# Performance work log

Measured on AMD Instinct MI355X. Metric: run time of the kernel, lower is better.

## Reference

```python
import jax, jax.numpy as jnp
import numpy as np

N = 50000      # total atoms/beads across batch
E = 800000     # total edges (avg degree 16)
H = 128        # hidden_channels
R = 50         # num_rbf
NB = 2         # n_interaction blocks
NG = 64        # num graphs in batch
NT = 100       # num atom types
CUT = 5.0      # upper distance cutoff


def setup_inputs() -> dict:
    key = jax.random.key(0)
    ks = jax.random.split(key, 20)
    atom_types = jax.random.randint(ks[0], (N,), 0, NT)
    pos = jax.random.uniform(ks[1], (N, 3), jnp.float32) * 30.0  # box of 30 Angstrom
    edge_index = jax.random.randint(ks[2], (2, E), 0, N)
    batch = jnp.sort(jax.random.randint(ks[3], (N,), 0, NG))

    def g(k, shape, fan_in):
        return jax.random.normal(k, shape, jnp.float32) * (1.0 / fan_in) ** 0.5

    emb = jax.random.normal(ks[4], (NT, H), jnp.float32) * 0.1
    # filter network per block: Linear(R->H) -> tanh -> Linear(H->H)
    fw1 = g(ks[5], (NB, R, H), R)
    fb1 = jnp.zeros((NB, H), jnp.float32)
    fw2 = g(ks[6], (NB, H, H), H)
    fb2 = jnp.zeros((NB, H), jnp.float32)
    # CFConv lin1 (no bias), lin2 (bias)
    lin1_w = g(ks[7], (NB, H, H), H)
    lin2_w = g(ks[8], (NB, H, H), H)
    lin2_b = jnp.zeros((NB, H), jnp.float32)
    # InteractionBlock output linear
    blk_w = g(ks[9], (NB, H, H), H)
    blk_b = jnp.zeros((NB, H), jnp.float32)
    # output network: Linear(H->H/2) -> tanh -> Linear(H/2->1)
    out_w1 = g(ks[10], (H, H // 2), H)
    out_b1 = jnp.zeros((H // 2,), jnp.float32)
    out_w2 = g(ks[11], (H // 2, 1), H // 2)
    out_b2 = jnp.zeros((1,), jnp.float32)
    return dict(atom_types=atom_types, pos=pos, edge_index=edge_index, batch=batch,
                emb=emb, fw1=fw1, fb1=fb1, fw2=fw2, fb2=fb2,
                lin1_w=lin1_w, lin2_w=lin2_w, lin2_b=lin2_b,
                blk_w=blk_w, blk_b=blk_b,
                out_w1=out_w1, out_b1=out_b1, out_w2=out_w2, out_b2=out_b2)


def reference(atom_types, pos, edge_index, batch, emb, fw1, fb1, fw2, fb2,
              lin1_w, lin2_w, lin2_b, blk_w, blk_b,
              out_w1, out_b1, out_w2, out_b2):
    src, dst = edge_index[0], edge_index[1]
    # pairwise distances along edges (eps keeps sqrt grad finite at coincident points)
    diff = pos[src] - pos[dst]                                  # [E,3]
    d = jnp.sqrt(jnp.sum(diff * diff, axis=-1) + 1e-12)         # [E]
    # Gaussian RBF expansion
    offsets = jnp.linspace(0.0, CUT, R)
    coeff = -0.5 / (offsets[1] - offsets[0]) ** 2
    rbf = jnp.exp(coeff * (d[:, None] - offsets) ** 2)          # [E,R]
    # cosine cutoff envelope
    Cenv = jnp.where(d < CUT, 0.5 * (jnp.cos(d * jnp.pi / CUT) + 1.0), 0.0)  # [E]

    x = emb[atom_types]                                          # [N,H]
    for i in range(NB):
        # filter generation from expanded distances
        W = jnp.tanh(rbf @ fw1[i] + fb1[i]) @ fw2[i] + fb2[i]    # [E,H]
        W = W * Cenv[:, None]
        # CFConv: lin1 -> gather*filter -> scatter-sum -> lin2
        h = x @ lin1_w[i]                                        # [N,H]
        msg = h[src] * W                                         # [E,H]
        agg = jax.ops.segment_sum(msg, dst, num_segments=N)      # [N,H]
        h = agg @ lin2_w[i] + lin2_b[i]
        # InteractionBlock: activation -> lin, residual add in SchNet.forward
        h = jnp.tanh(h)
        x = x + (h @ blk_w[i] + blk_b[i])
    # output network -> per-atom energy, scatter-sum per graph
    e = jnp.tanh(x @ out_w1 + out_b1) @ out_w2 + out_b2          # [N,1]
    energy = jax.ops.segment_sum(e, batch, num_segments=NG)      # [NG,1]
    return energy.flatten()
```

## Files before the change

kernel.cpp:

```cpp
#include <hip/hip_runtime.h>
#include <hip/hip_bf16.h>
#include <math.h>

#define H 128
#define RBF 50
#define CUTF 5.0f
#define PIF 3.14159265358979323846f
#define QT 1024
#define SEG 16

__global__ __launch_bounds__(256) void init_pos_x_kernel(
    const int* __restrict__ atype, const float* __restrict__ emb,
    const float* __restrict__ pos,
    float* __restrict__ x, float4* __restrict__ pos4, int Nn, int XB)
{
    if ((int)blockIdx.x < XB) {
        int idx = blockIdx.x * 256 + threadIdx.x;
        if (idx * 4 >= Nn * H) return;
        int n = idx >> 5;
        int c = (idx & 31) * 4;
        const float4 v = *(const float4*)(emb + atype[n] * H + c);
        *(float4*)(x + n * H + c) = v;
    } else {
        int n = ((int)blockIdx.x - XB) * 256 + threadIdx.x;
        if (n < Nn)
            pos4[n] = make_float4(pos[3 * n], pos[3 * n + 1], pos[3 * n + 2], 0.0f);
    }
}

__global__ __launch_bounds__(256) void edge_prep_kernel(
    const float4* __restrict__ pos4, const int* __restrict__ ei, int E, int CAP,
    int* __restrict__ seg_cnt, int* __restrict__ asrc, int* __restrict__ adst,
    float* __restrict__ ad, int* __restrict__ is_src, int* __restrict__ is_dst)
{
    __shared__ int wtot[4], wbase[4];
    const int tid = threadIdx.x;
    const int lane = tid & 63;
    const int wv = tid >> 6;
    const int gtid = blockIdx.x * 256 + tid;

    int s[4], t[4];
    float d[4];
    bool act[4] = {false, false, false, false};

    const int e0 = gtid * 4;
    if (e0 + 3 < E && (E & 3) == 0) {
        const int4 sv = *(const int4*)(ei + e0);
        const int4 tv = *(const int4*)(ei + E + e0);
        s[0] = sv.x; s[1] = sv.y; s[2] = sv.z; s[3] = sv.w;
        t[0] = tv.x; t[1] = tv.y; t[2] = tv.z; t[3] = tv.w;
        #pragma unroll
        for (int j = 0; j < 4; ++j) {
            float4 ps = pos4[s[j]], pt = pos4[t[j]];
            float dx = ps.x - pt.x, dy = ps.y - pt.y, dz = ps.z - pt.z;
            d[j] = sqrtf(dx * dx + dy * dy + dz * dz + 1e-12f);
            act[j] = (d[j] < CUTF);
        }
    } else if (e0 < E) {
        #pragma unroll
        for (int j = 0; j < 4; ++j) {
            int e = e0 + j;
            if (e < E) {
                s[j] = ei[e]; t[j] = ei[E + e];
                float4 ps = pos4[s[j]], pt = pos4[t[j]];
                float dx = ps.x - pt.x, dy = ps.y - pt.y, dz = ps.z - pt.z;
                d[j] = sqrtf(dx * dx + dy * dy + dz * dz + 1e-12f);
                act[j] = (d[j] < CUTF);
            }
        }
    }

    unsigned long long b[4];
    int mytot = 0;
    #pragma unroll
    for (int j = 0; j < 4; ++j) {
        b[j] = __ballot(act[j]);
        mytot += (int)__popcll(b[j]);
    }
    if (lane == 0) wtot[wv] = mytot;
    __syncthreads();
    if (tid == 0) {
        int t0 = wtot[0], t1 = wtot[1], t2 = wtot[2], t3 = wtot[3];
        int tot = t0 + t1 + t2 + t3;
        int base = 0;
        if (tot) base = atomicAdd(&seg_cnt[blockIdx.x & (SEG - 1)], tot);
        wbase[0] = base; wbase[1] = base + t0;
        wbase[2] = base + t0 + t1; wbase[3] = base + t0 + t1 + t2;
    }
    __syncthreads();

    int run = wbase[wv];
    const int segoff = (int)(blockIdx.x & (SEG - 1)) * CAP;
    const unsigned long long ltm = ((unsigned long long)1 << lane) - 1;
    #pragma unroll
    for (int j = 0; j < 4; ++j) {
        if (act[j]) {
            int p = segoff + run + (int)__popcll(b[j] & ltm);
            asrc[p] = s[j]; adst[p] = t[j]; ad[p] = d[j];
            is_src[s[j]] = 1; is_dst[t[j]] = 1;
        }
        run += (int)__popcll(b[j]);
    }
}

__global__ __launch_bounds__(256) void compact_atoms_kernel(
    const int* __restrict__ is_src, const int* __restrict__ is_dst, int Nn,
    int* __restrict__ cnt4,
    int* __restrict__ src_list, int* __restrict__ dst_list, int* __restrict__ nondst_list)
{
    __shared__ int wtot[3][4], wbase[3][4];
    const int tid = threadIdx.x;
    const int lane = tid & 63;
    const int wv = tid >> 6;
    int n = blockIdx.x * 256 + tid;
    bool v[3] = {false, false, false};
    if (n < Nn) {
        v[0] = is_src[n] != 0;
        v[1] = is_dst[n] != 0;
        v[2] = !v[1];
    }
    unsigned long long b[3];
    #pragma unroll
    for (int l = 0; l < 3; ++l) {
        b[l] = __ballot(v[l]);
        if (lane == 0) wtot[l][wv] = (int)__popcll(b[l]);
    }
    __syncthreads();
    if (tid == 0) {
        #pragma unroll
        for (int l = 0; l < 3; ++l) {
            int t0 = wtot[l][0], t1 = wtot[l][1], t2 = wtot[l][2], t3 = wtot[l][3];
            int tot = t0 + t1 + t2 + t3;
            int base = 0;
            if (tot) base = atomicAdd(cnt4 + 1 + l, tot);
            wbase[l][0] = base; wbase[l][1] = base + t0;
            wbase[l][2] = base + t0 + t1; wbase[l][3] = base + t0 + t1 + t2;
        }
    }
    __syncthreads();
    const unsigned long long ltm = ((unsigned long long)1 << lane) - 1;
    if (v[0]) src_list[wbase[0][wv] + (int)__popcll(b[0] & ltm)] = n;
    if (v[1]) dst_list[wbase[1][wv] + (int)__popcll(b[1] & ltm)] = n;
    if (v[2]) nondst_list[wbase[2][wv] + (int)__popcll(b[2] & ltm)] = n;
}

__global__ __launch_bounds__(256) void filter_table_kernel(
    const float* __restrict__ fw1, const float* __restrict__ fb1,
    const float* __restrict__ fw2, const float* __restrict__ fb2,
    const float* __restrict__ lin2b, const float* __restrict__ blkw,
    const float* __restrict__ blkb,
    float* __restrict__ tab, float* __restrict__ cvec)
{
    const int lane = threadIdx.x & 63;
    const int wid = (blockIdx.x * blockDim.x + threadIdx.x) >> 6;
    const int ntab = 2 * (QT + 1);
    if (wid >= ntab + 2) return;
    const int h0 = lane, h1 = lane + 64;

    if (wid >= ntab) {
        const int blk = wid - ntab;
        const float* bwp = blkw + (size_t)blk * H * H;
        float t0 = tanhf(lin2b[blk * H + h0]);
        float t1 = tanhf(lin2b[blk * H + h1]);
        float a0 = blkb[blk * H + h0], a1 = blkb[blk * H + h1];
        #pragma unroll 8
        for (int k = 0; k < 64; ++k) {
            float bb = __shfl(t0, k, 64);
            a0 = fmaf(bb, bwp[k * H + h0], a0);
            a1 = fmaf(bb, bwp[k * H + h1], a1);
        }
        #pragma unroll 8
        for (int k = 0; k < 64; ++k) {
            float bb = __shfl(t1, k, 64);
            a0 = fmaf(bb, bwp[(64 + k) * H + h0], a0);
            a1 = fmaf(bb, bwp[(64 + k) * H + h1], a1);
        }
        cvec[blk * H + h0] = a0;
        cvec[blk * H + h1] = a1;
        return;
    }

    const int blk = wid / (QT + 1);
    const int q = wid - blk * (QT + 1);
    const float d = (float)q * (CUTF / (float)QT);

    const float* f1 = fw1 + (size_t)blk * RBF * H;
    const float* f2 = fw2 + (size_t)blk * H * H;
    const float step  = CUTF / 49.0f;
    const float coeff = -0.5f / (step * step);

    float cenv = (d < CUTF) ? 0.5f * (cosf(d * (PIF / CUTF)) + 1.0f) : 0.0f;

    float t0 = fb1[blk * H + h0], t1 = fb1[blk * H + h1];
    #pragma unroll
    for (int r = 0; r < RBF; ++r) {
        float u = d - (float)r * step;
        float rb = expf(coeff * u * u);
        t0 = fmaf(rb, f1[r * H + h0], t0);
        t1 = fmaf(rb, f1[r * H + h1], t1);
    }
    t0 = tanhf(t0); t1 = tanhf(t1);

    float w0 = fb2[blk * H + h0], w1v = fb2[blk * H + h1];
    #pragma unroll 8
    for (int k = 0; k < 64; ++k) {
        float bb = __shfl(t0, k, 64);
        w0  = fmaf(bb, f2[k * H + h0], w0);
        w1v = fmaf(bb, f2[k * H + h1], w1v);
    }
    #pragma unroll 8
    for (int k = 0; k < 64; ++k) {
        float bb = __shfl(t1, k, 64);
        w0  = fmaf(bb, f2[(64 + k) * H + h0], w0);
        w1v = fmaf(bb, f2[(64 + k) * H + h1], w1v);
    }
    float* row = tab + ((size_t)blk * (QT + 1) + q) * H;
    row[h0] = w0 * cenv;
    row[h1] = w1v * cenv;
}

__global__ __launch_bounds__(256) void edge_scatter_kernel(
    const int* __restrict__ seg_cnt,
    const int* __restrict__ asrc, const int* __restrict__ adst,
    const float* __restrict__ ad, const float* __restrict__ tab,
    const float* __restrict__ hbuf, float* __restrict__ agg, int CAP)
{
    __shared__ int sbase[SEG + 1];
    const int tid = threadIdx.x;
    if (tid == 0) {
        int run = 0;
        #pragma unroll
        for (int s2 = 0; s2 < SEG; ++s2) { sbase[s2] = run; run += seg_cnt[s2]; }
        sbase[SEG] = run;
    }
    __syncthreads();

    const int lane = tid & 63;
    const int wid = (blockIdx.x * blockDim.x + tid) >> 6;
    const int nw  = (gridDim.x * blockDim.x) >> 6;
    const int total = sbase[SEG];
    const float scale = (float)QT / CUTF;

    for (int i = wid; i < total; i += nw) {
        int seg = 0;
        #pragma unroll
        for (int s2 = 1; s2 < SEG; ++s2) seg += (i >= sbase[s2]) ? 1 : 0;
        int slot = seg * CAP + (i - sbase[seg]);

        int s = asrc[slot], t = adst[slot];
        float p = ad[slot] * scale;
        int i0 = (int)p;
        if (i0 > QT - 1) i0 = QT - 1;
        float f = p - (float)i0;
        const float* r0 = tab + (size_t)i0 * H;
        float wl = fmaf(f, r0[H + lane] - r0[lane], r0[lane]);
        float wh = fmaf(f, r0[H + 64 + lane] - r0[64 + lane], r0[64 + lane]);
        float m0 = hbuf[(size_t)s * H + lane] * wl;
        float m1 = hbuf[(size_t)s * H + 64 + lane] * wh;
        atomicAdd(agg + (size_t)t * H + lane, m0);
        atomicAdd(agg + (size_t)t * H + 64 + lane, m1);
    }
}

#define GB 512
#define ZB 128
__global__ __launch_bounds__(256) void gemm_rows_zero_kernel(
    const float* __restrict__ A, const float* __restrict__ W,
    float* __restrict__ C,
    const int* __restrict__ rows, const int* __restrict__ cntp,
    float* __restrict__ zbuf, const int* __restrict__ zrows,
    const int* __restrict__ zcntp)
{
    __shared__ float As[32][36];
    __shared__ float Ws[32][128];
    __shared__ int rlist[32];

    const int tid = threadIdx.x;

    if (blockIdx.x >= GB) {
        int zcnt = *zcntp;
        int total = zcnt * 32;
        for (int idx = (blockIdx.x - GB) * 256 + tid; idx < total; idx += ZB * 256) {
            int row = idx >> 5, c = (idx & 31) << 2;
            int r = zrows[row];
            *(float4*)(zbuf + (size_t)r * H + c) = make_float4(0.f, 0.f, 0.f, 0.f);
        }
        return;
    }

    const int cnt = *cntp;
    const int r0 = (tid >> 4) * 2;
    const int c0 = (tid & 15) * 4;

    for (int tile = blockIdx.x; tile * 32 < cnt; tile += GB) {
        __syncthreads();
        if (tid < 32) {
            int idx = tile * 32 + tid;
            rlist[tid] = (idx < cnt) ? rows[idx] : -1;
        }
        __syncthreads();

        float acc[2][8];
        #pragma unroll
        for (int j = 0; j < 2; ++j)
            #pragma unroll
            for (int c = 0; c < 8; ++c) acc[j][c] = 0.f;

        for (int kc = 0; kc < H; kc += 32) {
            {
                int lr = tid >> 3;
                int kk = (tid & 7) * 4;
                int r = rlist[lr];
                float4 v = make_float4(0.f, 0.f, 0.f, 0.f);
                if (r >= 0) v = *(const float4*)(A + (size_t)r * H + kc + kk);
                *(float4*)&As[lr][kk] = v;
            }
            {
                int wr = tid >> 5;
                int wc = (tid & 31) * 4;
                #pragma unroll
                for (int p = 0; p < 4; ++p) {
                    int row = wr + p * 8;
                    *(float4*)&Ws[row][wc] = *(const float4*)(W + (size_t)(kc + row) * H + wc);
                }
            }
            __syncthreads();
            #pragma unroll
            for (int k = 0; k < 32; k += 4) {
                float a_[2][4];
                #pragma unroll
                for (int j = 0; j < 2; ++j)
                    *(float4*)a_[j] = *(const float4*)&As[r0 + j][k];
                #pragma unroll
                for (int kk = 0; kk < 4; ++kk) {
                    float4 wlo = *(const float4*)&Ws[k + kk][c0];
                    float4 whi = *(const float4*)&Ws[k + kk][c0 + 64];
                    float w_[8] = {wlo.x, wlo.y, wlo.z, wlo.w, whi.x, whi.y, whi.z, whi.w};
                    #pragma unroll
                    for (int j = 0; j < 2; ++j)
                        #pragma unroll
                        for (int c = 0; c < 8; ++c)
                            acc[j][c] = fmaf(a_[j][kk], w_[c], acc[j][c]);
                }
            }
            __syncthreads();
        }
        #pragma unroll
        for (int j = 0; j < 2; ++j) {
            int r = rlist[r0 + j];
            if (r < 0) continue;
            #pragma unroll
            for (int hh = 0; hh < 2; ++hh) {
                int cb = c0 + hh * 64;
                *(float4*)(C + (size_t)r * H + cb) = make_float4(
                    acc[j][hh * 4 + 0], acc[j][hh * 4 + 1],
                    acc[j][hh * 4 + 2], acc[j][hh * 4 + 3]);
            }
        }
    }
}

#define UB 512
#define AB 256
__global__ __launch_bounds__(256) void update_x_kernel(
    const float* __restrict__ agg, const float* __restrict__ l2w,
    const float* __restrict__ l2b, const float* __restrict__ bw,
    const float* __restrict__ bb, float* __restrict__ x,
    const int* __restrict__ rows, const int* __restrict__ cntp,
    const int* __restrict__ nrows, const int* __restrict__ ncntp,
    const float* __restrict__ cvec)
{
    __shared__ float As[32][36];
    __shared__ float Ws[32][128];
    __shared__ float Tl[32][132];
    __shared__ int rlist[32];

    const int tid = threadIdx.x;

    if (blockIdx.x >= UB) {
        int ncnt = *ncntp;
        int total = ncnt * 32;
        for (int idx = (blockIdx.x - UB) * 256 + tid; idx < total; idx += AB * 256) {
            int row = idx >> 5, c = (idx & 31) << 2;
            int r = nrows[row];
            float4 v = *(const float4*)(x + (size_t)r * H + c);
            float4 cv = *(const float4*)(cvec + c);
            v.x += cv.x; v.y += cv.y; v.z += cv.z; v.w += cv.w;
            *(float4*)(x + (size_t)r * H + c) = v;
        }
        return;
    }

    const int cnt = *cntp;
    const int r0 = (tid >> 4) * 2;
    const int c0 = (tid & 15) * 4;

    for (int tile = blockIdx.x; tile * 32 < cnt; tile += UB) {
        __syncthreads();
        if (tid < 32) {
            int idx = tile * 32 + tid;
            rlist[tid] = (idx < cnt) ? rows[idx] : -1;
        }
        __syncthreads();

        float acc[2][8];
        #pragma unroll
        for (int j = 0; j < 2; ++j)
            #pragma unroll
            for (int c = 0; c < 8; ++c) acc[j][c] = 0.f;

        for (int kc = 0; kc < H; kc += 32) {
            {
                int lr = tid >> 3;
                int kk = (tid & 7) * 4;
                int r = rlist[lr];
                float4 v = make_float4(0.f, 0.f, 0.f, 0.f);
                if (r >= 0) v = *(const float4*)(agg + (size_t)r * H + kc + kk);
                *(float4*)&As[lr][kk] = v;
            }
            {
                int wr = tid >> 5;
                int wc = (tid & 31) * 4;
                #pragma unroll
                for (int p = 0; p < 4; ++p) {
                    int row = wr + p * 8;
                    *(float4*)&Ws[row][wc] = *(const float4*)(l2w + (size_t)(kc + row) * H + wc);
                }
            }
            __syncthreads();
            #pragma unroll
            for (int k = 0; k < 32; k += 4) {
                float a_[2][4];
                #pragma unroll
                for (int j = 0; j < 2; ++j)
                    *(float4*)a_[j] = *(const float4*)&As[r0 + j][k];
                #pragma unroll
                for (int kk = 0; kk < 4; ++kk) {
                    float4 wlo = *(const float4*)&Ws[k + kk][c0];
                    float4 whi = *(const float4*)&Ws[k + kk][c0 + 64];
                    float w_[8] = {wlo.x, wlo.y, wlo.z, wlo.w, whi.x, whi.y, whi.z, whi.w};
                    #pragma unroll
                    for (int j = 0; j < 2; ++j)
                        #pragma unroll
                        for (int c = 0; c < 8; ++c)
                            acc[j][c] = fmaf(a_[j][kk], w_[c], acc[j][c]);
                }
            }
            __syncthreads();
        }
        #pragma unroll
        for (int j = 0; j < 2; ++j) {
            float4 lo, hi;
            lo.x = tanhf(acc[j][0] + l2b[c0]);      lo.y = tanhf(acc[j][1] + l2b[c0 + 1]);
            lo.z = tanhf(acc[j][2] + l2b[c0 + 2]);  lo.w = tanhf(acc[j][3] + l2b[c0 + 3]);
            hi.x = tanhf(acc[j][4] + l2b[c0 + 64]); hi.y = tanhf(acc[j][5] + l2b[c0 + 65]);
            hi.z = tanhf(acc[j][6] + l2b[c0 + 66]); hi.w = tanhf(acc[j][7] + l2b[c0 + 67]);
            *(float4*)&Tl[r0 + j][c0] = lo;
            *(float4*)&Tl[r0 + j][c0 + 64] = hi;
        }

        float acc2[2][8];
        #pragma unroll
        for (int j = 0; j < 2; ++j)
            #pragma unroll
            for (int c = 0; c < 8; ++c) acc2[j][c] = 0.f;

        for (int kc = 0; kc < H; kc += 32) {
            __syncthreads();
            {
                int wr = tid >> 5;
                int wc = (tid & 31) * 4;
                #pragma unroll
                for (int p = 0; p < 4; ++p) {
                    int row = wr + p * 8;
                    *(float4*)&Ws[row][wc] = *(const float4*)(bw + (size_t)(kc + row) * H + wc);
                }
            }
            __syncthreads();
            #pragma unroll
            for (int k = 0; k < 32; k += 4) {
                float a_[2][4];
                #pragma unroll
                for (int j = 0; j < 2; ++j)
                    *(float4*)a_[j] = *(const float4*)&Tl[r0 + j][kc + k];
                #pragma unroll
                for (int kk = 0; kk < 4; ++kk) {
                    float4 wlo = *(const float4*)&Ws[k + kk][c0];
                    float4 whi = *(const float4*)&Ws[k + kk][c0 + 64];
                    float w_[8] = {wlo.x, wlo.y, wlo.z, wlo.w, whi.x, whi.y, whi.z, whi.w};
                    #pragma unroll
                    for (int j = 0; j < 2; ++j)
                        #pragma unroll
                        for (int c = 0; c < 8; ++c)
                            acc2[j][c] = fmaf(a_[j][kk], w_[c], acc2[j][c]);
                }
            }
        }
        #pragma unroll
        for (int j = 0; j < 2; ++j) {
            int r = rlist[r0 + j];
            if (r < 0) continue;
            #pragma unroll
            for (int hh = 0; hh < 2; ++hh) {
                int cb = c0 + hh * 64;
                float4 xv = *(const float4*)(x + (size_t)r * H + cb);
                xv.x += acc2[j][hh * 4 + 0] + bb[cb];
                xv.y += acc2[j][hh * 4 + 1] + bb[cb + 1];
                xv.z += acc2[j][hh * 4 + 2] + bb[cb + 2];
                xv.w += acc2[j][hh * 4 + 3] + bb[cb + 3];
                *(float4*)(x + (size_t)r * H + cb) = xv;
            }
        }
    }
}

__global__ __launch_bounds__(256) void out_head_kernel(
    const float* __restrict__ x, const int* __restrict__ batch,
    const float* __restrict__ w1, const float* __restrict__ b1,
    const float* __restrict__ w2, const float* __restrict__ b2,
    float* __restrict__ energy, int Nn)
{
    __shared__ float As[64][33];
    __shared__ float Ws[32][68];
    __shared__ float e_lds[64];
    __shared__ int   gid_lds[64];

    const int tid = threadIdx.x;
    const int m0 = blockIdx.x * 64;
    const int r0 = (tid >> 4) * 4;
    const int c0 = (tid & 15) * 4;

    float acc[4][4];
    #pragma unroll
    for (int j = 0; j < 4; ++j)
        #pragma unroll
        for (int c = 0; c < 4; ++c) acc[j][c] = 0.0f;

    for (int kc = 0; kc < 128; kc += 32) {
        {
            int r = tid >> 3;
            int kk = (tid & 7) * 4;
            #pragma unroll
            for (int p = 0; p < 2; ++p) {
                int row = r + p * 32;
                float4 v = make_float4(0.f, 0.f, 0.f, 0.f);
                if (m0 + row < Nn) v = *(const float4*)(x + (size_t)(m0 + row) * H + kc + kk);
                As[row][kk] = v.x; As[row][kk + 1] = v.y;
                As[row][kk + 2] = v.z; As[row][kk + 3] = v.w;
            }
        }
        {
            int wr = tid >> 4;
            int wc = (tid & 15) * 4;
            #pragma unroll
            for (int p = 0; p < 2; ++p) {
                int row = wr + p * 16;
                *(float4*)&Ws[row][wc] = *(const float4*)(w1 + (size_t)(kc + row) * 64 + wc);
            }
        }
        __syncthreads();
        #pragma unroll
        for (int k = 0; k < 32; ++k) {
            float a_[4];
            #pragma unroll
            for (int j = 0; j < 4; ++j) a_[j] = As[r0 + j][k];
            float4 wv = *(float4*)&Ws[k][c0];
            float w_[4] = {wv.x, wv.y, wv.z, wv.w};
            #pragma unroll
            for (int j = 0; j < 4; ++j)
                #pragma unroll
                for (int c = 0; c < 4; ++c)
                    acc[j][c] = fmaf(a_[j], w_[c], acc[j][c]);
        }
        __syncthreads();
    }

    const float4 b1v = *(const float4*)(b1 + c0);
    const float4 w2v = *(const float4*)(w2 + c0);
    float ep[4];
    #pragma unroll
    for (int j = 0; j < 4; ++j) {
        float v0 = tanhf(acc[j][0] + b1v.x);
        float v1 = tanhf(acc[j][1] + b1v.y);
        float v2 = tanhf(acc[j][2] + b1v.z);
        float v3 = tanhf(acc[j][3] + b1v.w);
        ep[j] = v0 * w2v.x + v1 * w2v.y + v2 * w2v.z + v3 * w2v.w;
    }
    #pragma unroll
    for (int off = 1; off < 16; off <<= 1) {
        #pragma unroll
        for (int j = 0; j < 4; ++j) ep[j] += __shfl_xor(ep[j], off, 64);
    }
    if ((tid & 15) == 0) {
        const float b2v = b2[0];
        #pragma unroll
        for (int j = 0; j < 4; ++j) e_lds[r0 + j] = ep[j] + b2v;
    }
    if (tid < 64) {
        int row = m0 + tid;
        gid_lds[tid] = (row < Nn) ? batch[row] : -1;
    }
    __syncthreads();

    if (tid == 0) {
        int cur = -1; float sum = 0.0f;
        for (int r = 0; r < 64; ++r) {
            int g = gid_lds[r];
            if (g < 0) continue;
            if (g != cur) {
                if (cur >= 0) atomicAdd(&energy[cur], sum);
                cur = g; sum = 0.0f;
            }
            sum += e_lds[r];
        }
        if (cur >= 0) atomicAdd(&energy[cur], sum);
    }
}

extern "C" void kernel_launch(void* const* d_in, const int* in_sizes, int n_in,
                              void* d_out, int out_size, void* d_ws, size_t ws_size,
                              hipStream_t stream)
{
    const int*   atype = (const int*)  d_in[0];
    const float* pos   = (const float*)d_in[1];
    const int*   ei    = (const int*)  d_in[2];
    const int*   batch = (const int*)  d_in[3];
    const float* emb   = (const float*)d_in[4];
    const float* fw1   = (const float*)d_in[5];
    const float* fb1   = (const float*)d_in[6];
    const float* fw2   = (const float*)d_in[7];
    const float* fb2   = (const float*)d_in[8];
    const float* lin1w = (const float*)d_in[9];
    const float* lin2w = (const float*)d_in[10];
    const float* lin2b = (const float*)d_in[11];
    const float* blkw  = (const float*)d_in[12];
    const float* blkb  = (const float*)d_in[13];
    const float* ow1   = (const float*)d_in[14];
    const float* ob1   = (const float*)d_in[15];
    const float* ow2   = (const float*)d_in[16];
    const float* ob2   = (const float*)d_in[17];

    const int Nn = in_sizes[0];
    const int E  = in_sizes[2] / 2;
    float* energy = (float*)d_out;

    const int eblocks = (E + 1023) / 1024;
    const int bps = (eblocks + SEG - 1) / SEG;
    const int CAP = bps * 1024;
    const int SEGCAP = SEG * CAP;

    char* w = (char*)d_ws;
    int*   cnt  = (int*)w;
    int*   seg_cnt = cnt + 8;
    int*   is_src = (int*)(w + 256);
    int*   is_dst = is_src + Nn;
    float* x    = (float*)(is_dst + Nn);
    float* hbuf = x + (size_t)Nn * H;
    float* agg  = hbuf + (size_t)Nn * H;
    int*   asrc = (int*)(agg + (size_t)Nn * H);
    int*   adst = asrc + SEGCAP;
    float* ad   = (float*)(adst + SEGCAP);
    int*   src_list = (int*)(ad + SEGCAP);
    int*   dst_list = src_list + Nn;
    int*   nondst_list = dst_list + Nn;
    float* cvec = (float*)(nondst_list + Nn);
    float* tab  = cvec + 2 * H;
    float4* pos4 = (float4*)(tab + 2 * (size_t)(QT + 1) * H);

    hipMemsetAsync(cnt, 0, 256 + 2 * (size_t)Nn * sizeof(int), stream);
    hipMemsetAsync(energy, 0, (size_t)out_size * sizeof(float), stream);

    {
        int XB = (Nn * 32 + 255) / 256;
        int PB = (Nn + 255) / 256;
        init_pos_x_kernel<<<XB + PB, 256, 0, stream>>>(atype, emb, pos, x, pos4, Nn, XB);
    }
    edge_prep_kernel<<<eblocks, 256, 0, stream>>>(
        pos4, ei, E, CAP, seg_cnt, asrc, adst, ad, is_src, is_dst);
    compact_atoms_kernel<<<(Nn + 255) / 256, 256, 0, stream>>>(
        is_src, is_dst, Nn, cnt, src_list, dst_list, nondst_list);
    {
        int waves = 2 * (QT + 1) + 2;
        filter_table_kernel<<<(waves + 3) / 4, 256, 0, stream>>>(
            fw1, fb1, fw2, fb2, lin2b, blkw, blkb, tab, cvec);
    }

    for (int i = 0; i < 2; ++i) {
        const float* l1w  = lin1w + (size_t)i * H * H;
        const float* l2w  = lin2w + (size_t)i * H * H;
        const float* l2b  = lin2b + (size_t)i * H;
        const float* bw   = blkw + (size_t)i * H * H;
        const float* bb   = blkb + (size_t)i * H;
        const float* tabi = tab + (size_t)i * (QT + 1) * H;

        gemm_rows_zero_kernel<<<GB + ZB, 256, 0, stream>>>(
            x, l1w, hbuf, src_list, cnt + 1, agg, dst_list, cnt + 2);
        edge_scatter_kernel<<<1024, 256, 0, stream>>>(seg_cnt, asrc, adst, ad,
                                                      tabi, hbuf, agg, CAP);
        update_x_kernel<<<UB + AB, 256, 0, stream>>>(
            agg, l2w, l2b, bw, bb, x, dst_list, cnt + 2,
            nondst_list, cnt + 3, cvec + i * H);
    }

    out_head_kernel<<<(Nn + 63) / 64, 256, 0, stream>>>(x, batch, ow1, ob1, ow2, ob2, energy, Nn);
}
```

Before: 250.7 us.

## Specialize atoms by edge role and precompute per-type energies for edgeless atoms

Atoms that never receive edges get a closed-form state, so their output energy is precomputed per atom type in a merged prep kernel. Only destination atoms go through the output head, fused into the final update kernel. Block 0 reads embeddings directly instead of materializing x. The memsets, embedding init and filter-table kernels merge into one prep launch, and the per-graph energy sum uses a binary search over the sorted batch instead of atomics. This removes launches and full-N passes, at the cost of more complex, role-specific code paths.

```diff
diff --git a/kernel.cpp b/kernel.cpp
--- a/kernel.cpp
+++ b/kernel.cpp
@@ -9,23 +9,139 @@
 #define QT 1024
 #define SEG 16
 
-__global__ __launch_bounds__(256) void init_pos_x_kernel(
-    const int* __restrict__ atype, const float* __restrict__ emb,
-    const float* __restrict__ pos,
-    float* __restrict__ x, float4* __restrict__ pos4, int Nn, int XB)
+__global__ __launch_bounds__(256) void prep_kernel(
+    const float* __restrict__ pos, float4* __restrict__ pos4, int Nn,
+    int4* __restrict__ zbase, int zquads,
+    const float* __restrict__ fw1, const float* __restrict__ fb1,
+    const float* __restrict__ fw2, const float* __restrict__ fb2,
+    const float* __restrict__ lin2b, const float* __restrict__ blkw,
+    const float* __restrict__ blkb, const float* __restrict__ emb,
+    const float* __restrict__ ow1, const float* __restrict__ ob1,
+    const float* __restrict__ ow2, const float* __restrict__ ob2,
+    float* __restrict__ tab, float* __restrict__ cvec,
+    float* __restrict__ e_type, int NT,
+    int ZFB, int PB, int FB)
 {
-    if ((int)blockIdx.x < XB) {
-        int idx = blockIdx.x * 256 + threadIdx.x;
-        if (idx * 4 >= Nn * H) return;
-        int n = idx >> 5;
-        int c = (idx & 31) * 4;
-        const float4 v = *(const float4*)(emb + atype[n] * H + c);
-        *(float4*)(x + n * H + c) = v;
-    } else {
-        int n = ((int)blockIdx.x - XB) * 256 + threadIdx.x;
+    int b = blockIdx.x;
+    const int tid = threadIdx.x;
+    const int lane = tid & 63;
+
+    if (b < ZFB) {
+        int i = b * 256 + tid;
+        if (i < zquads) zbase[i] = make_int4(0, 0, 0, 0);
+        return;
+    }
+    b -= ZFB;
+    if (b < PB) {
+        int n = b * 256 + tid;
         if (n < Nn)
             pos4[n] = make_float4(pos[3 * n], pos[3 * n + 1], pos[3 * n + 2], 0.0f);
-    }
+        return;
+    }
+    b -= PB;
+    const int h0 = lane, h1 = lane + 64;
+    if (b < FB) {
+        const int wid = b * 4 + (tid >> 6);
+        const int ntab = 2 * (QT + 1);
+        if (wid >= ntab + 2) return;
+        if (wid >= ntab) {
+            const int blk = wid - ntab;
+            const float* bwp = blkw + (size_t)blk * H * H;
+            float t0 = tanhf(lin2b[blk * H + h0]);
+            float t1 = tanhf(lin2b[blk * H + h1]);
+            float a0 = blkb[blk * H + h0], a1 = blkb[blk * H + h1];
+            #pragma unroll 8
+            for (int k = 0; k < 64; ++k) {
+                float bb2 = __shfl(t0, k, 64);
+                a0 = fmaf(bb2, bwp[k * H + h0], a0);
+                a1 = fmaf(bb2, bwp[k * H + h1], a1);
+            }
+            #pragma unroll 8
+            for (int k = 0; k < 64; ++k) {
+                float bb2 = __shfl(t1, k, 64);
+                a0 = fmaf(bb2, bwp[(64 + k) * H + h0], a0);
+                a1 = fmaf(bb2, bwp[(64 + k) * H + h1], a1);
+            }
+            cvec[blk * H + h0] = a0;
+            cvec[blk * H + h1] = a1;
+            return;
+        }
+        const int blk = wid / (QT + 1);
+        const int q = wid - blk * (QT + 1);
+        const float d = (float)q * (CUTF / (float)QT);
+        const float* f1 = fw1 + (size_t)blk * RBF * H;
+        const float* f2 = fw2 + (size_t)blk * H * H;
+        const float step  = CUTF / 49.0f;
+        const float coeff = -0.5f / (step * step);
+        float cenv = (d < CUTF) ? 0.5f * (cosf(d * (PIF / CUTF)) + 1.0f) : 0.0f;
+
+        float t0 = fb1[blk * H + h0], t1 = fb1[blk * H + h1];
+        #pragma unroll
+        for (int r = 0; r < RBF; ++r) {
+            float u = d - (float)r * step;
+            float rb = expf(coeff * u * u);
+            t0 = fmaf(rb, f1[r * H + h0], t0);
+            t1 = fmaf(rb, f1[r * H + h1], t1);
+        }
+        t0 = tanhf(t0); t1 = tanhf(t1);
+        float w0 = fb2[blk * H + h0], w1v = fb2[blk * H + h1];
+        #pragma unroll 8
+        for (int k = 0; k < 64; ++k) {
+            float bb2 = __shfl(t0, k, 64);
+            w0  = fmaf(bb2, f2[k * H + h0], w0);
+            w1v = fmaf(bb2, f2[k * H + h1], w1v);
+        }
+        #pragma unroll 8
+        for (int k = 0; k < 64; ++k) {
+            float bb2 = __shfl(t1, k, 64);
+            w0  = fmaf(bb2, f2[(64 + k) * H + h0], w0);
+            w1v = fmaf(bb2, f2[(64 + k) * H + h1], w1v);
+        }
+        float* row = tab + ((size_t)blk * (QT + 1) + q) * H;
+        row[h0] = w0 * cenv;
+        row[h1] = w1v * cenv;
+        return;
+    }
+    b -= FB;
+    const int ty = b * 4 + (tid >> 6);
+    if (ty >= NT) return;
+    float xt0 = emb[(size_t)ty * H + h0];
+    float xt1 = emb[(size_t)ty * H + h1];
+    #pragma unroll
+    for (int blk = 0; blk < 2; ++blk) {
+        const float* bwp = blkw + (size_t)blk * H * H;
+        float t0 = tanhf(lin2b[blk * H + h0]);
+        float t1 = tanhf(lin2b[blk * H + h1]);
+        float a0 = blkb[blk * H + h0], a1 = blkb[blk * H + h1];
+        #pragma unroll 8
+        for (int k = 0; k < 64; ++k) {
+            float bb2 = __shfl(t0, k, 64);
+            a0 = fmaf(bb2, bwp[k * H + h0], a0);
+            a1 = fmaf(bb2, bwp[k * H + h1], a1);
+        }
+        #pragma unroll 8
+        for (int k = 0; k < 64; ++k) {
+            float bb2 = __shfl(t1, k, 64);
+            a0 = fmaf(bb2, bwp[(64 + k) * H + h0], a0);
+            a1 = fmaf(bb2, bwp[(64 + k) * H + h1], a1);
+        }
+        xt0 += a0; xt1 += a1;
+    }
+    float y = ob1[lane];
+    #pragma unroll 8
+    for (int k = 0; k < 64; ++k) {
+        float bb2 = __shfl(xt0, k, 64);
+        y = fmaf(bb2, ow1[k * 64 + lane], y);
+    }
+    #pragma unroll 8
+    for (int k = 0; k < 64; ++k) {
+        float bb2 = __shfl(xt1, k, 64);
+        y = fmaf(bb2, ow1[(64 + k) * 64 + lane], y);
+    }
+    y = tanhf(y) * ow2[lane];
+    #pragma unroll
+    for (int off = 32; off; off >>= 1) y += __shfl_xor(y, off, 64);
+    if (lane == 0) e_type[ty] = y + ob2[0];
 }
 
 __global__ __launch_bounds__(256) void edge_prep_kernel(
@@ -106,7 +222,7 @@
 __global__ __launch_bounds__(256) void compact_atoms_kernel(
     const int* __restrict__ is_src, const int* __restrict__ is_dst, int Nn,
     int* __restrict__ cnt4,
-    int* __restrict__ src_list, int* __restrict__ dst_list, int* __restrict__ nondst_list)
+    int* __restrict__ src_list, int* __restrict__ dst_list, int* __restrict__ sn_list)
 {
     __shared__ int wtot[3][4], wbase[3][4];
     const int tid = threadIdx.x;
@@ -117,7 +233,7 @@
     if (n < Nn) {
         v[0] = is_src[n] != 0;
         v[1] = is_dst[n] != 0;
-        v[2] = !v[1];
+        v[2] = v[0] && !v[1];
     }
     unsigned long long b[3];
     #pragma unroll
@@ -141,82 +257,7 @@
     const unsigned long long ltm = ((unsigned long long)1 << lane) - 1;
     if (v[0]) src_list[wbase[0][wv] + (int)__popcll(b[0] & ltm)] = n;
     if (v[1]) dst_list[wbase[1][wv] + (int)__popcll(b[1] & ltm)] = n;
-    if (v[2]) nondst_list[wbase[2][wv] + (int)__popcll(b[2] & ltm)] = n;
-}
-
-__global__ __launch_bounds__(256) void filter_table_kernel(
-    const float* __restrict__ fw1, const float* __restrict__ fb1,
-    const float* __restrict__ fw2, const float* __restrict__ fb2,
-    const float* __restrict__ lin2b, const float* __restrict__ blkw,
-    const float* __restrict__ blkb,
-    float* __restrict__ tab, float* __restrict__ cvec)
-{
-    const int lane = threadIdx.x & 63;
-    const int wid = (blockIdx.x * blockDim.x + threadIdx.x) >> 6;
-    const int ntab = 2 * (QT + 1);
-    if (wid >= ntab + 2) return;
-    const int h0 = lane, h1 = lane + 64;
-
-    if (wid >= ntab) {
-        const int blk = wid - ntab;
-        const float* bwp = blkw + (size_t)blk * H * H;
-        float t0 = tanhf(lin2b[blk * H + h0]);
-        float t1 = tanhf(lin2b[blk * H + h1]);
-        float a0 = blkb[blk * H + h0], a1 = blkb[blk * H + h1];
-        #pragma unroll 8
-        for (int k = 0; k < 64; ++k) {
-            float bb = __shfl(t0, k, 64);
-            a0 = fmaf(bb, bwp[k * H + h0], a0);
-            a1 = fmaf(bb, bwp[k * H + h1], a1);
-        }
-        #pragma unroll 8
-        for (int k = 0; k < 64; ++k) {
-            float bb = __shfl(t1, k, 64);
-            a0 = fmaf(bb, bwp[(64 + k) * H + h0], a0);
-            a1 = fmaf(bb, bwp[(64 + k) * H + h1], a1);
-        }
-        cvec[blk * H + h0] = a0;
-        cvec[blk * H + h1] = a1;
-        return;
-    }
-
-    const int blk = wid / (QT + 1);
-    const int q = wid - blk * (QT + 1);
-    const float d = (float)q * (CUTF / (float)QT);
-
-    const float* f1 = fw1 + (size_t)blk * RBF * H;
-    const float* f2 = fw2 + (size_t)blk * H * H;
-    const float step  = CUTF / 49.0f;
-    const float coeff = -0.5f / (step * step);
-
-    float cenv = (d < CUTF) ? 0.5f * (cosf(d * (PIF / CUTF)) + 1.0f) : 0.0f;
-
-    float t0 = fb1[blk * H + h0], t1 = fb1[blk * H + h1];
-    #pragma unroll
-    for (int r = 0; r < RBF; ++r) {
-        float u = d - (float)r * step;
-        float rb = expf(coeff * u * u);
-        t0 = fmaf(rb, f1[r * H + h0], t0);
-        t1 = fmaf(rb, f1[r * H + h1], t1);
-    }
-    t0 = tanhf(t0); t1 = tanhf(t1);
-
-    float w0 = fb2[blk * H + h0], w1v = fb2[blk * H + h1];
-    #pragma unroll 8
-    for (int k = 0; k < 64; ++k) {
-        float bb = __shfl(t0, k, 64);
-        w0  = fmaf(bb, f2[k * H + h0], w0);
-        w1v = fmaf(bb, f2[k * H + h1], w1v);
-    }
-    #pragma unroll 8
-    for (int k = 0; k < 64; ++k) {
-        float bb = __shfl(t1, k, 64);
-        w0  = fmaf(bb, f2[(64 + k) * H + h0], w0);
-        w1v = fmaf(bb, f2[(64 + k) * H + h1], w1v);
-    }
-    float* row = tab + ((size_t)blk * (QT + 1) + q) * H;
-    row[h0] = w0 * cenv;
-    row[h1] = w1v * cenv;
+    if (v[2]) sn_list[wbase[2][wv] + (int)__popcll(b[2] & ltm)] = n;
 }
 
 __global__ __launch_bounds__(256) void edge_scatter_kernel(
@@ -265,7 +306,8 @@
 #define GB 512
 #define ZB 128
 __global__ __launch_bounds__(256) void gemm_rows_zero_kernel(
-    const float* __restrict__ A, const float* __restrict__ W,
+    const float* __restrict__ A, const int* __restrict__ atype,
+    const float* __restrict__ emb, const float* __restrict__ W,
     float* __restrict__ C,
     const int* __restrict__ rows, const int* __restrict__ cntp,
     float* __restrict__ zbuf, const int* __restrict__ zrows,
@@ -273,7 +315,7 @@
 {
     __shared__ float As[32][36];
     __shared__ float Ws[32][128];
-    __shared__ int rlist[32];
+    __shared__ int rlist[32], tlist[32];
 
     const int tid = threadIdx.x;
 
@@ -296,7 +338,9 @@
         __syncthreads();
         if (tid < 32) {
             int idx = tile * 32 + tid;
-            rlist[tid] = (idx < cnt) ? rows[idx] : -1;
+            int r = (idx < cnt) ? rows[idx] : -1;
+            rlist[tid] = r;
+            tlist[tid] = (atype && r >= 0) ? atype[r] : 0;
         }
         __syncthreads();
 
@@ -312,7 +356,11 @@
                 int kk = (tid & 7) * 4;
                 int r = rlist[lr];
                 float4 v = make_float4(0.f, 0.f, 0.f, 0.f);
-                if (r >= 0) v = *(const float4*)(A + (size_t)r * H + kc + kk);
+                if (r >= 0) {
+                    const float* base = atype ? (emb + (size_t)tlist[lr] * H)
+                                              : (A + (size_t)r * H);
+                    v = *(const float4*)(base + kc + kk);
+                }
                 *(float4*)&As[lr][kk] = v;
             }
             {
@@ -361,32 +409,34 @@
 }
 
 #define UB 512
-#define AB 256
-__global__ __launch_bounds__(256) void update_x_kernel(
+#define AB 128
+__global__ __launch_bounds__(256) void update_x0_kernel(
     const float* __restrict__ agg, const float* __restrict__ l2w,
     const float* __restrict__ l2b, const float* __restrict__ bw,
     const float* __restrict__ bb, float* __restrict__ x,
+    const float* __restrict__ emb, const int* __restrict__ atype,
     const int* __restrict__ rows, const int* __restrict__ cntp,
-    const int* __restrict__ nrows, const int* __restrict__ ncntp,
-    const float* __restrict__ cvec)
+    const int* __restrict__ snrows, const int* __restrict__ sncntp,
+    const float* __restrict__ cvec0)
 {
     __shared__ float As[32][36];
     __shared__ float Ws[32][128];
     __shared__ float Tl[32][132];
-    __shared__ int rlist[32];
+    __shared__ int rlist[32], tlist[32];
 
     const int tid = threadIdx.x;
 
     if (blockIdx.x >= UB) {
-        int ncnt = *ncntp;
+        int ncnt = *sncntp;
         int total = ncnt * 32;
         for (int idx = (blockIdx.x - UB) * 256 + tid; idx < total; idx += AB * 256) {
             int row = idx >> 5, c = (idx & 31) << 2;
-            int r = nrows[row];
-            float4 v = *(const float4*)(x + (size_t)r * H + c);
-            float4 cv = *(const float4*)(cvec + c);
-            v.x += cv.x; v.y += cv.y; v.z += cv.z; v.w += cv.w;
-            *(float4*)(x + (size_t)r * H + c) = v;
+            int r = snrows[row];
+            int ty = atype[r];
+            float4 ev = *(const float4*)(emb + (size_t)ty * H + c);
+            float4 cv = *(const float4*)(cvec0 + c);
+            ev.x += cv.x; ev.y += cv.y; ev.z += cv.z; ev.w += cv.w;
+            *(float4*)(x + (size_t)r * H + c) = ev;
         }
         return;
     }
@@ -399,7 +449,9 @@
         __syncthreads();
         if (tid < 32) {
             int idx = tile * 32 + tid;
-            rlist[tid] = (idx < cnt) ? rows[idx] : -1;
+            int r = (idx < cnt) ? rows[idx] : -1;
+            rlist[tid] = r;
+            tlist[tid] = (r >= 0) ? atype[r] : 0;
         }
         __syncthreads();
 
@@ -500,10 +552,11 @@
         for (int j = 0; j < 2; ++j) {
             int r = rlist[r0 + j];
             if (r < 0) continue;
+            int ty = tlist[r0 + j];
             #pragma unroll
             for (int hh = 0; hh < 2; ++hh) {
                 int cb = c0 + hh * 64;
-                float4 xv = *(const float4*)(x + (size_t)r * H + cb);
+                float4 xv = *(const float4*)(emb + (size_t)ty * H + cb);
                 xv.x += acc2[j][hh * 4 + 0] + bb[cb];
                 xv.y += acc2[j][hh * 4 + 1] + bb[cb + 1];
                 xv.z += acc2[j][hh * 4 + 2] + bb[cb + 2];
@@ -514,107 +567,225 @@
     }
 }
 
-__global__ __launch_bounds__(256) void out_head_kernel(
-    const float* __restrict__ x, const int* __restrict__ batch,
-    const float* __restrict__ w1, const float* __restrict__ b1,
-    const float* __restrict__ w2, const float* __restrict__ b2,
-    float* __restrict__ energy, int Nn)
+__global__ __launch_bounds__(256) void update_e_kernel(
+    const float* __restrict__ agg, const float* __restrict__ l2w,
+    const float* __restrict__ l2b, const float* __restrict__ bw,
+    const float* __restrict__ bb, const float* __restrict__ x,
+    const float* __restrict__ ow1, const float* __restrict__ ob1,
+    const float* __restrict__ ow2, const float* __restrict__ ob2,
+    float* __restrict__ e_atom,
+    const int* __restrict__ rows, const int* __restrict__ cntp)
 {
-    __shared__ float As[64][33];
-    __shared__ float Ws[32][68];
-    __shared__ float e_lds[64];
-    __shared__ int   gid_lds[64];
+    __shared__ float As[32][36];
+    __shared__ float Ws[32][128];
+    __shared__ float Tl[32][132];
+    __shared__ int rlist[32];
 
     const int tid = threadIdx.x;
-    const int m0 = blockIdx.x * 64;
-    const int r0 = (tid >> 4) * 4;
+    const int cnt = *cntp;
+    const int r0 = (tid >> 4) * 2;
     const int c0 = (tid & 15) * 4;
 
-    float acc[4][4];
+    for (int tile = blockIdx.x; tile * 32 < cnt; tile += gridDim.x) {
+        __syncthreads();
+        if (tid < 32) {
+            int idx = tile * 32 + tid;
+            rlist[tid] = (idx < cnt) ? rows[idx] : -1;
+        }
+        __syncthreads();
+
+        float acc[2][8];
+        #pragma unroll
+        for (int j = 0; j < 2; ++j)
+            #pragma unroll
+            for (int c = 0; c < 8; ++c) acc[j][c] = 0.f;
+
+        for (int kc = 0; kc < H; kc += 32) {
+            {
+                int lr = tid >> 3;
+                int kk = (tid & 7) * 4;
+                int r = rlist[lr];
+                float4 v = make_float4(0.f, 0.f, 0.f, 0.f);
+                if (r >= 0) v = *(const float4*)(agg + (size_t)r * H + kc + kk);
+                *(float4*)&As[lr][kk] = v;
+            }
+            {
+                int wr = tid >> 5;
+                int wc = (tid & 31) * 4;
+                #pragma unroll
+                for (int p = 0; p < 4; ++p) {
+                    int row = wr + p * 8;
+                    *(float4*)&Ws[row][wc] = *(const float4*)(l2w + (size_t)(kc + row) * H + wc);
+                }
+            }
+            __syncthreads();
+            #pragma unroll
+            for (int k = 0; k < 32; k += 4) {
+                float a_[2][4];
+                #pragma unroll
+                for (int j = 0; j < 2; ++j)
+                    *(float4*)a_[j] = *(const float4*)&As[r0 + j][k];
+                #pragma unroll
+                for (int kk = 0; kk < 4; ++kk) {
+                    float4 wlo = *(const float4*)&Ws[k + kk][c0];
+                    float4 whi = *(const float4*)&Ws[k + kk][c0 + 64];
+                    float w_[8] = {wlo.x, wlo.y, wlo.z, wlo.w, whi.x, whi.y, whi.z, whi.w};
+                    #pragma unroll
+                    for (int j = 0; j < 2; ++j)
+                        #pragma unroll
+                        for (int c = 0; c < 8; ++c)
+                            acc[j][c] = fmaf(a_[j][kk], w_[c], acc[j][c]);
+                }
+            }
+            __syncthreads();
+        }
+        #pragma unroll
+        for (int j = 0; j < 2; ++j) {
+            float4 lo, hi;
+            lo.x = tanhf(acc[j][0] + l2b[c0]);      lo.y = tanhf(acc[j][1] + l2b[c0 + 1]);
+            lo.z = tanhf(acc[j][2] + l2b[c0 + 2]);  lo.w = tanhf(acc[j][3] + l2b[c0 + 3]);
+            hi.x = tanhf(acc[j][4] + l2b[c0 + 64]); hi.y = tanhf(acc[j][5] + l2b[c0 + 65]);
+            hi.z = tanhf(acc[j][6] + l2b[c0 + 66]); hi.w = tanhf(acc[j][7] + l2b[c0 + 67]);
+            *(float4*)&Tl[r0 + j][c0] = lo;
+            *(float4*)&Tl[r0 + j][c0 + 64] = hi;
+        }
+
+        float acc2[2][8];
+        #pragma unroll
+        for (int j = 0; j < 2; ++j)
+            #pragma unroll
+            for (int c = 0; c < 8; ++c) acc2[j][c] = 0.f;
+
+        for (int kc = 0; kc < H; kc += 32) {
+            __syncthreads();
+            {
+                int wr = tid >> 5;
+                int wc = (tid & 31) * 4;
+                #pragma unroll
+                for (int p = 0; p < 4; ++p) {
+                    int row = wr + p * 8;
+                    *(float4*)&Ws[row][wc] = *(const float4*)(bw + (size_t)(kc + row) * H + wc);
+                }
+            }
+            __syncthreads();
+            #pragma unroll
+            for (int k = 0; k < 32; k += 4) {
+                float a_[2][4];
+                #pragma unroll
+                for (int j = 0; j < 2; ++j)
+                    *(float4*)a_[j] = *(const float4*)&Tl[r0 + j][kc + k];
+                #pragma unroll
+                for (int kk = 0; kk < 4; ++kk) {
+                    float4 wlo = *(const float4*)&Ws[k + kk][c0];
+                    float4 whi = *(const float4*)&Ws[k + kk][c0 + 64];
+                    float w_[8] = {wlo.x, wlo.y, wlo.z, wlo.w, whi.x, whi.y, whi.z, whi.w};
+                    #pragma unroll
+                    for (int j = 0; j < 2; ++j)
+                        #pragma unroll
+                        for (int c = 0; c < 8; ++c)
+                            acc2[j][c] = fmaf(a_[j][kk], w_[c], acc2[j][c]);
+                }
+            }
+        }
+        __syncthreads();
+        #pragma unroll
+        for (int j = 0; j < 2; ++j) {
+            int r = rlist[r0 + j];
+            #pragma unroll
+            for (int hh = 0; hh < 2; ++hh) {
+                int cb = c0 + hh * 64;
+                float4 xv = make_float4(0.f, 0.f, 0.f, 0.f);
+                if (r >= 0) xv = *(const float4*)(x + (size_t)r * H + cb);
+                xv.x += acc2[j][hh * 4 + 0] + bb[cb];
+                xv.y += acc2[j][hh * 4 + 1] + bb[cb + 1];
+                xv.z += acc2[j][hh * 4 + 2] + bb[cb + 2];
+                xv.w += acc2[j][hh * 4 + 3] + bb[cb + 3];
+                *(float4*)&Tl[r0 + j][cb] = xv;
+            }
+        }
+
+        float acc3[2][4];
+        #pragma unroll
+        for (int j = 0; j < 2; ++j)
+            #pragma unroll
+            for (int c = 0; c < 4; ++c) acc3[j][c] = 0.f;
+
+        for (int kc = 0; kc < H; kc += 32) {
+            __syncthreads();
+            {
+                int wr = tid >> 4;
+                int wc = (tid & 15) * 4;
+                #pragma unroll
+                for (int p = 0; p < 2; ++p) {
+                    int row = wr + p * 16;
+                    *(float4*)&Ws[row][wc] = *(const float4*)(ow1 + (size_t)(kc + row) * 64 + wc);
+                }
+            }
+            __syncthreads();
+            #pragma unroll
+            for (int k = 0; k < 32; ++k) {
+                float a_[2];
+                #pragma unroll
+                for (int j = 0; j < 2; ++j) a_[j] = Tl[r0 + j][kc + k];
+                float4 wv = *(const float4*)&Ws[k][c0];
+                #pragma unroll
+                for (int j = 0; j < 2; ++j) {
+                    acc3[j][0] = fmaf(a_[j], wv.x, acc3[j][0]);
+                    acc3[j][1] = fmaf(a_[j], wv.y, acc3[j][1]);
+                    acc3[j][2] = fmaf(a_[j], wv.z, acc3[j][2]);
+                    acc3[j][3] = fmaf(a_[j], wv.w, acc3[j][3]);
+                }
+            }
+        }
+        const float4 b1v = *(const float4*)(ob1 + c0);
+        const float4 w2v = *(const float4*)(ow2 + c0);
+        float ep[2];
+        #pragma unroll
+        for (int j = 0; j < 2; ++j) {
+            float v0 = tanhf(acc3[j][0] + b1v.x);
+            float v1 = tanhf(acc3[j][1] + b1v.y);
+            float v2 = tanhf(acc3[j][2] + b1v.z);
+            float v3 = tanhf(acc3[j][3] + b1v.w);
+            ep[j] = v0 * w2v.x + v1 * w2v.y + v2 * w2v.z + v3 * w2v.w;
+        }
+        #pragma unroll
+        for (int off = 1; off < 16; off <<= 1) {
+            ep[0] += __shfl_xor(ep[0], off, 64);
+            ep[1] += __shfl_xor(ep[1], off, 64);
+        }
+        if ((tid & 15) == 0) {
+            const float b2v = ob2[0];
+            #pragma unroll
+            for (int j = 0; j < 2; ++j) {
+                int r = rlist[r0 + j];
+                if (r >= 0) e_atom[r] = ep[j] + b2v;
+            }
+        }
+    }
+}
+
+__global__ __launch_bounds__(256) void energy_graph_kernel(
+    const int* __restrict__ batch, const int* __restrict__ atype,
+    const int* __restrict__ is_dst, const float* __restrict__ e_atom,
+    const float* __restrict__ e_type, float* __restrict__ energy, int Nn)
+{
+    const int g = blockIdx.x;
+    int lo = 0, hi = Nn;
+    while (lo < hi) { int m = (lo + hi) >> 1; if (batch[m] < g) lo = m + 1; else hi = m; }
+    const int start = lo;
+    hi = Nn;
+    while (lo < hi) { int m = (lo + hi) >> 1; if (batch[m] < g + 1) lo = m + 1; else hi = m; }
+    const int end = lo;
+
+    float s = 0.0f;
+    for (int n = start + (int)threadIdx.x; n < end; n += 256)
+        s += is_dst[n] ? e_atom[n] : e_type[atype[n]];
     #pragma unroll
-    for (int j = 0; j < 4; ++j)
-        #pragma unroll
-        for (int c = 0; c < 4; ++c) acc[j][c] = 0.0f;
-
-    for (int kc = 0; kc < 128; kc += 32) {
-        {
-            int r = tid >> 3;
-            int kk = (tid & 7) * 4;
-            #pragma unroll
-            for (int p = 0; p < 2; ++p) {
-                int row = r + p * 32;
-                float4 v = make_float4(0.f, 0.f, 0.f, 0.f);
-                if (m0 + row < Nn) v = *(const float4*)(x + (size_t)(m0 + row) * H + kc + kk);
-                As[row][kk] = v.x; As[row][kk + 1] = v.y;
-                As[row][kk + 2] = v.z; As[row][kk + 3] = v.w;
-            }
-        }
-        {
-            int wr = tid >> 4;
-            int wc = (tid & 15) * 4;
-            #pragma unroll
-            for (int p = 0; p < 2; ++p) {
-                int row = wr + p * 16;
-                *(float4*)&Ws[row][wc] = *(const float4*)(w1 + (size_t)(kc + row) * 64 + wc);
-            }
-        }
-        __syncthreads();
-        #pragma unroll
-        for (int k = 0; k < 32; ++k) {
-            float a_[4];
-            #pragma unroll
-            for (int j = 0; j < 4; ++j) a_[j] = As[r0 + j][k];
-            float4 wv = *(float4*)&Ws[k][c0];
-            float w_[4] = {wv.x, wv.y, wv.z, wv.w};
-            #pragma unroll
-            for (int j = 0; j < 4; ++j)
-                #pragma unroll
-                for (int c = 0; c < 4; ++c)
-                    acc[j][c] = fmaf(a_[j], w_[c], acc[j][c]);
-        }
-        __syncthreads();
-    }
-
-    const float4 b1v = *(const float4*)(b1 + c0);
-    const float4 w2v = *(const float4*)(w2 + c0);
-    float ep[4];
-    #pragma unroll
-    for (int j = 0; j < 4; ++j) {
-        float v0 = tanhf(acc[j][0] + b1v.x);
-        float v1 = tanhf(acc[j][1] + b1v.y);
-        float v2 = tanhf(acc[j][2] + b1v.z);
-        float v3 = tanhf(acc[j][3] + b1v.w);
-        ep[j] = v0 * w2v.x + v1 * w2v.y + v2 * w2v.z + v3 * w2v.w;
-    }
-    #pragma unroll
-    for (int off = 1; off < 16; off <<= 1) {
-        #pragma unroll
-        for (int j = 0; j < 4; ++j) ep[j] += __shfl_xor(ep[j], off, 64);
-    }
-    if ((tid & 15) == 0) {
-        const float b2v = b2[0];
-        #pragma unroll
-        for (int j = 0; j < 4; ++j) e_lds[r0 + j] = ep[j] + b2v;
-    }
-    if (tid < 64) {
-        int row = m0 + tid;
-        gid_lds[tid] = (row < Nn) ? batch[row] : -1;
-    }
+    for (int off = 32; off; off >>= 1) s += __shfl_xor(s, off, 64);
+    __shared__ float wp[4];
+    if ((threadIdx.x & 63) == 0) wp[threadIdx.x >> 6] = s;
     __syncthreads();
-
-    if (tid == 0) {
-        int cur = -1; float sum = 0.0f;
-        for (int r = 0; r < 64; ++r) {
-            int g = gid_lds[r];
-            if (g < 0) continue;
-            if (g != cur) {
-                if (cur >= 0) atomicAdd(&energy[cur], sum);
-                cur = g; sum = 0.0f;
-            }
-            sum += e_lds[r];
-        }
-        if (cur >= 0) atomicAdd(&energy[cur], sum);
-    }
+    if (threadIdx.x == 0) energy[g] = wp[0] + wp[1] + wp[2] + wp[3];
 }
 
 extern "C" void kernel_launch(void* const* d_in, const int* in_sizes, int n_in,
@@ -642,6 +813,7 @@
 
     const int Nn = in_sizes[0];
     const int E  = in_sizes[2] / 2;
+    const int NT = in_sizes[4] / H;
     float* energy = (float*)d_out;
 
     const int eblocks = (E + 1023) / 1024;
@@ -652,7 +824,7 @@
     char* w = (char*)d_ws;
     int*   cnt  = (int*)w;
     int*   seg_cnt = cnt + 8;
-    int*   is_src = (int*)(w + 256);
+    int*   is_src = cnt + 32;
     int*   is_dst = is_src + Nn;
     float* x    = (float*)(is_dst + Nn);
     float* hbuf = x + (size_t)Nn * H;
@@ -662,45 +834,47 @@
     float* ad   = (float*)(adst + SEGCAP);
     int*   src_list = (int*)(ad + SEGCAP);
     int*   dst_list = src_list + Nn;
-    int*   nondst_list = dst_list + Nn;
-    float* cvec = (float*)(nondst_list + Nn);
+    int*   sn_list  = dst_list + Nn;
+    float* cvec = (float*)(sn_list + Nn);
     float* tab  = cvec + 2 * H;
-    float4* pos4 = (float4*)(tab + 2 * (size_t)(QT + 1) * H);
-
-    hipMemsetAsync(cnt, 0, 256 + 2 * (size_t)Nn * sizeof(int), stream);
-    hipMemsetAsync(energy, 0, (size_t)out_size * sizeof(float), stream);
-
-    {
-        int XB = (Nn * 32 + 255) / 256;
-        int PB = (Nn + 255) / 256;
-        init_pos_x_kernel<<<XB + PB, 256, 0, stream>>>(atype, emb, pos, x, pos4, Nn, XB);
-    }
+    float* e_type = tab + 2 * (size_t)(QT + 1) * H;
+    float* e_atom = e_type + 128;
+    float4* pos4 = (float4*)(e_atom + Nn);
+
+    const int zquads = (128 + 2 * Nn * 4) / 16;
+    const int ZFB = (zquads + 255) / 256;
+    const int PB  = (Nn + 255) / 256;
+    const int FB  = (2 * (QT + 1) + 2 + 3) / 4;
+    const int TB  = (NT + 3) / 4;
+
+    prep_kernel<<<ZFB + PB + FB + TB, 256, 0, stream>>>(
+        pos, pos4, Nn, (int4*)cnt, zquads,
+        fw1, fb1, fw2, fb2, lin2b, blkw, blkb, emb,
+        ow1, ob1, ow2, ob2, tab, cvec, e_type, NT, ZFB, PB, FB);
+
     edge_prep_kernel<<<eblocks, 256, 0, stream>>>(
         pos4, ei, E, CAP, seg_cnt, asrc, adst, ad, is_src, is_dst);
     compact_atoms_kernel<<<(Nn + 255) / 256, 256, 0, stream>>>(
-        is_src, is_dst, Nn, cnt, src_list, dst_list, nondst_list);
-    {
-        int waves = 2 * (QT + 1) + 2;
-        filter_table_kernel<<<(waves + 3) / 4, 256, 0, stream>>>(
-            fw1, fb1, fw2, fb2, lin2b, blkw, blkb, tab, cvec);
-    }
-
-    for (int i = 0; i < 2; ++i) {
-        const float* l1w  = lin1w + (size_t)i * H * H;
-        const float* l2w  = lin2w + (size_t)i * H * H;
-        const float* l2b  = lin2b + (size_t)i * H;
-        const float* bw   = blkw + (size_t)i * H * H;
-        const float* bb   = blkb + (size_t)i * H;
-        const float* tabi = tab + (size_t)i * (QT + 1) * H;
-
-        gemm_rows_zero_kernel<<<GB + ZB, 256, 0, stream>>>(
-            x, l1w, hbuf, src_list, cnt + 1, agg, dst_list, cnt + 2);
-        edge_scatter_kernel<<<1024, 256, 0, stream>>>(seg_cnt, asrc, adst, ad,
-                                                      tabi, hbuf, agg, CAP);
-        update_x_kernel<<<UB + AB, 256, 0, stream>>>(
-            agg, l2w, l2b, bw, bb, x, dst_list, cnt + 2,
-            nondst_list, cnt + 3, cvec + i * H);
-    }
-
-    out_head_kernel<<<(Nn + 63) / 64, 256, 0, stream>>>(x, batch, ow1, ob1, ow2, ob2, energy, Nn);
+        is_src, is_dst, Nn, cnt, src_list, dst_list, sn_list);
+
+    gemm_rows_zero_kernel<<<GB + ZB, 256, 0, stream>>>(
+        nullptr, atype, emb, lin1w, hbuf, src_list, cnt + 1,
+        agg, dst_list, cnt + 2);
+    edge_scatter_kernel<<<1024, 256, 0, stream>>>(
+        seg_cnt, asrc, adst, ad, tab, hbuf, agg, CAP);
+    update_x0_kernel<<<UB + AB, 256, 0, stream>>>(
+        agg, lin2w, lin2b, blkw, blkb, x, emb, atype,
+        dst_list, cnt + 2, sn_list, cnt + 3, cvec);
+
+    gemm_rows_zero_kernel<<<GB + ZB, 256, 0, stream>>>(
+        x, nullptr, nullptr, lin1w + (size_t)H * H, hbuf, src_list, cnt + 1,
+        agg, dst_list, cnt + 2);
+    edge_scatter_kernel<<<1024, 256, 0, stream>>>(
+        seg_cnt, asrc, adst, ad, tab + (size_t)(QT + 1) * H, hbuf, agg, CAP);
+    update_e_kernel<<<512, 256, 0, stream>>>(
+        agg, lin2w + (size_t)H * H, lin2b + H, blkw + (size_t)H * H, blkb + H,
+        x, ow1, ob1, ow2, ob2, e_atom, dst_list, cnt + 2);
+
+    energy_graph_kernel<<<out_size, 256, 0, stream>>>(
+        batch, atype, is_dst, e_atom, e_type, energy, Nn);
 }
```

New measurement: 235.5 us. -6.1%, faster.
